# Kernel optimization log

Measured on AMD Instinct MI355X. Metric: run time of the kernel, lower is better.

## Reference

```python
import jax, jax.numpy as jnp
import numpy as np

N_NODES = 50000


def setup_inputs() -> dict:
    key = jax.random.key(0)
    k1, k2, k3, k4 = jax.random.split(key, 4)
    x = jax.random.normal(k1, (N_NODES, 256), dtype=jnp.float32)
    edge_index = jax.random.randint(k2, (2, 800000), 0, N_NODES, dtype=jnp.int64)
    W1 = jax.random.normal(k3, (256, 128), dtype=jnp.float32) * (1.0 / np.sqrt(256))
    b1 = jnp.zeros((128,), dtype=jnp.float32)
    W2 = jax.random.normal(k4, (128, 16), dtype=jnp.float32) * (1.0 / np.sqrt(128))
    b2 = jnp.zeros((16,), dtype=jnp.float32)
    return {"x": x, "edge_index": edge_index, "W1": W1, "b1": b1, "W2": W2, "b2": b2}


def _gcn_norm(edge_index, num_nodes):
    # add self-loops, then symmetric normalization D^-1/2 A D^-1/2 (PyG GCNConv default)
    loop = jnp.arange(num_nodes, dtype=edge_index.dtype)
    src = jnp.concatenate([edge_index[0], loop])
    dst = jnp.concatenate([edge_index[1], loop])
    deg = jax.ops.segment_sum(jnp.ones_like(dst, dtype=jnp.float32), dst, num_segments=num_nodes)
    dinv = jnp.where(deg > 0, jax.lax.rsqrt(deg), 0.0)
    norm = dinv[src] * dinv[dst]  # [E+N]
    return src, dst, norm


def _gcn_conv(h, W, b, src, dst, norm, num_nodes):
    h = h @ W                             # linear before propagate
    msg = h[src] * norm[:, None]          # gather + edge scaling
    agg = jax.ops.segment_sum(msg, dst, num_segments=num_nodes)  # scatter-add
    return agg + b


def reference(x, edge_index, W1, b1, W2, b2):
    n = x.shape[0]
    src, dst, norm = _gcn_norm(edge_index, n)
    h = jax.nn.relu(_gcn_conv(x, W1, b1, src, dst, norm, n))
    # F.dropout(training=False) is identity in eval mode
    out = _gcn_conv(h, W2, b2, src, dst, norm, n)
    return jax.nn.log_softmax(out, axis=1)
```

## Files before the change

kernel.cpp:

```cpp
#include <hip/hip_runtime.h>
#include <hip/hip_bf16.h>
#include <math.h>


#define FIN 256
#define FH  128
#define FO  16
#define ECH_LOG 13
#define ECH (1 << ECH_LOG)
#define NCHUNK 98
#define WPH 6272

typedef unsigned int uint;
typedef unsigned short ushort;
typedef unsigned char uchar;
typedef __attribute__((ext_vector_type(8))) short bf16x8;
typedef __attribute__((ext_vector_type(4))) float f32x4;

static __device__ __forceinline__ ushort f2bf(float f) {
    __hip_bfloat16 b = __float2bfloat16(f);
    return *reinterpret_cast<ushort*>(&b);
}
static __device__ __forceinline__ float bf2f(ushort u) {
    return __uint_as_float(((uint)u) << 16);
}

__global__ __launch_bounds__(256) void GCN_wprep_k(const float* __restrict__ W1,
                                                   ushort* __restrict__ whT,
                                                   ushort* __restrict__ wlT) {
    int i = blockIdx.x * 256 + threadIdx.x;
    int k = i >> 7, c = i & 127;
    float w = W1[i];
    ushort hh = f2bf(w);
    ushort hl = f2bf(w - bf2f(hh));
    whT[c * 256 + k] = hh;
    wlT[c * 256 + k] = hl;
}

#define G1_BR 64
#define G1_KC 32

__global__ __launch_bounds__(256, 4) void GCN_histgemm_k(
        const float* __restrict__ x, const ushort* __restrict__ whT,
        const ushort* __restrict__ wlT, ushort* __restrict__ h1,
        const int* __restrict__ edge, uint* __restrict__ cw,
        uchar* __restrict__ rank8,
        int N, int E, int nHist, int nWords, int wph) {
    __shared__ __align__(16) char smem[WPH * 4];
    int tid = threadIdx.x;

    if ((int)blockIdx.x < nHist) {
        int bid = blockIdx.x;
        int half = bid & 1;
        int c = bid >> 1;
        uint* lh = (uint*)smem;
        int w0 = half * wph;
        int wlim = nWords - w0; if (wlim > wph) wlim = wph;
        for (int j = tid; j < wlim; j += 256) lh[j] = 0;
        __syncthreads();
        int base = c << ECH_LOG;
        int lim = base + ECH; if (lim > E) lim = E;
        for (int i = base + tid; i < lim; i += 256) {
            int d = edge[E + i];
            int wd = (d >> 2) - w0;
            if ((unsigned)wd < (unsigned)wlim) {
                int sh = (d & 3) << 3;
                uint old = atomicAdd(&lh[wd], 1u << sh);
                rank8[i] = (uchar)((old >> sh) & 0xFFu);
            }
        }
        __syncthreads();
        for (int j = tid; j < wlim; j += 256)
            cw[(size_t)c * nWords + w0 + j] = lh[j];
        return;
    }

    ushort* xh_s = (ushort*)smem;
    ushort* wh_s = (ushort*)(smem + 4096);
    ushort* wl_s = (ushort*)(smem + 12288);
    int row0 = (blockIdx.x - nHist) * G1_BR;
    int ln = tid & 63;
    int w  = tid >> 6;
    int ln15 = ln & 15;
    int q16  = ln >> 4;

    f32x4 acc[4][2];
    #pragma unroll
    for (int mr = 0; mr < 4; mr++)
        #pragma unroll
        for (int nc = 0; nc < 2; nc++) acc[mr][nc] = (f32x4){0.f, 0.f, 0.f, 0.f};

    for (int kc = 0; kc < FIN; kc += G1_KC) {
        #pragma unroll
        for (int j = 0; j < 2; j++) {
            int u = tid + j * 256;
            int r = u >> 3, kq = u & 7;
            int gr = row0 + r;
            float4 v = make_float4(0.f, 0.f, 0.f, 0.f);
            if (gr < N) v = *(const float4*)&x[(size_t)gr * FIN + kc + kq * 4];
            uint2 hw;
            hw.x = (uint)f2bf(v.x) | ((uint)f2bf(v.y) << 16);
            hw.y = (uint)f2bf(v.z) | ((uint)f2bf(v.w) << 16);
            int byte = (r * 64 + kq * 8) ^ (((r >> 1) & 3) << 4);
            *(uint2*)((char*)xh_s + byte) = hw;
        }
        #pragma unroll
        for (int j = 0; j < 2; j++) {
            int u = tid + j * 256;
            int c = u >> 2, ku = u & 3;
            uint4 vh = *(const uint4*)&whT[(size_t)c * 256 + kc + ku * 8];
            uint4 vl = *(const uint4*)&wlT[(size_t)c * 256 + kc + ku * 8];
            int byte = (c * 64 + ku * 16) ^ (((c >> 1) & 3) << 4);
            *(uint4*)((char*)wh_s + byte) = vh;
            *(uint4*)((char*)wl_s + byte) = vl;
        }
        __syncthreads();

        bf16x8 ah[4], bh[2], bl[2];
        #pragma unroll
        for (int mr = 0; mr < 4; mr++) {
            int r = mr * 16 + ln15;
            int byte = r * 64 + ((q16 * 16) ^ (((r >> 1) & 3) << 4));
            ah[mr] = *(const bf16x8*)((const char*)xh_s + byte);
        }
        #pragma unroll
        for (int nc = 0; nc < 2; nc++) {
            int c = w * 32 + nc * 16 + ln15;
            int byte = c * 64 + ((q16 * 16) ^ (((c >> 1) & 3) << 4));
            bh[nc] = *(const bf16x8*)((const char*)wh_s + byte);
            bl[nc] = *(const bf16x8*)((const char*)wl_s + byte);
        }
        #pragma unroll
        for (int mr = 0; mr < 4; mr++)
            #pragma unroll
            for (int nc = 0; nc < 2; nc++) {
                acc[mr][nc] = __builtin_amdgcn_mfma_f32_16x16x32_bf16(
                    ah[mr], bh[nc], acc[mr][nc], 0, 0, 0);
                acc[mr][nc] = __builtin_amdgcn_mfma_f32_16x16x32_bf16(
                    ah[mr], bl[nc], acc[mr][nc], 0, 0, 0);
            }
        __syncthreads();
    }

    #pragma unroll
    for (int mr = 0; mr < 4; mr++) {
        #pragma unroll
        for (int nc = 0; nc < 2; nc++) {
            int cw2 = w * 32 + nc * 16 + ln15;
            #pragma unroll
            for (int j = 0; j < 4; j++) {
                int gr = row0 + mr * 16 + q16 * 4 + j;
                if (gr < N) h1[(size_t)gr * FH + cw2] = f2bf(acc[mr][nc][j]);
            }
        }
    }
}

__global__ __launch_bounds__(256) void GCN_chpfx_k(uint* __restrict__ cw,
                                                   int* __restrict__ count,
                                                   int* __restrict__ bsum,
                                                   int N, int nWords) {
    __shared__ int part[4][64][4];
    __shared__ int red[64];
    int tid = threadIdx.x;
    int wl = tid & 63, g = tid >> 6;
    int w = blockIdx.x * 64 + wl;
    int c0 = g * 25;
    int c1 = c0 + 25; if (c1 > NCHUNK) c1 = NCHUNK;

    int s0 = 0, s1 = 0, s2 = 0, s3 = 0;
    if (w < nWords) {
        for (int c = c0; c < c1; c++) {
            uint v = cw[(size_t)c * nWords + w];
            s0 += (int)(v & 0xFFu);
            s1 += (int)((v >> 8) & 0xFFu);
            s2 += (int)((v >> 16) & 0xFFu);
            s3 += (int)((v >> 24) & 0xFFu);
        }
    }
    part[g][wl][0] = s0; part[g][wl][1] = s1;
    part[g][wl][2] = s2; part[g][wl][3] = s3;
    __syncthreads();

    int b0 = 0, b1 = 0, b2 = 0, b3 = 0;
    for (int gg = 0; gg < g; gg++) {
        b0 += part[gg][wl][0]; b1 += part[gg][wl][1];
        b2 += part[gg][wl][2]; b3 += part[gg][wl][3];
    }
    if (w < nWords) {
        uint r0 = (uint)b0, r1 = (uint)b1, r2 = (uint)b2, r3 = (uint)b3;
        for (int c = c0; c < c1; c++) {
            uint* p = &cw[(size_t)c * nWords + w];
            uint v = *p;
            *p = (r0 & 0xFFu) | ((r1 & 0xFFu) << 8) | ((r2 & 0xFFu) << 16) | ((r3 & 0xFFu) << 24);
            r0 += v & 0xFFu;
            r1 += (v >> 8) & 0xFFu;
            r2 += (v >> 16) & 0xFFu;
            r3 += (v >> 24) & 0xFFu;
        }
    }
    int local = 0;
    if (g == 3 && w < nWords) {
        int t0 = b0 + s0, t1 = b1 + s1, t2 = b2 + s2, t3 = b3 + s3;
        int d0 = 4 * w;
        if (d0 + 0 < N) count[d0 + 0] = t0;
        if (d0 + 1 < N) count[d0 + 1] = t1;
        if (d0 + 2 < N) count[d0 + 2] = t2;
        if (d0 + 3 < N) count[d0 + 3] = t3;
        local = t0 + t1 + t2 + t3 + 4;
    }
    if (g == 3) red[wl] = local;
    __syncthreads();
    if (tid < 32) { red[tid] += red[tid + 32]; }
    __syncthreads();
    if (tid < 16) { red[tid] += red[tid + 16]; }
    __syncthreads();
    if (tid < 8) { red[tid] += red[tid + 8]; }
    __syncthreads();
    if (tid < 4) { red[tid] += red[tid + 4]; }
    __syncthreads();
    if (tid == 0) bsum[blockIdx.x] = red[0] + red[1] + red[2] + red[3];
}

__global__ __launch_bounds__(256) void GCN_scan2_k(const int* __restrict__ count,
                                                   const int* __restrict__ bsum,
                                                   int2* __restrict__ rd2,
                                                   uint* __restrict__ edata, int N) {
    int tid = threadIdx.x;
    int b = blockIdx.x;
    int d = b * 256 + tid;
    int cnt1 = (d < N) ? count[d] + 1 : 0;

    __shared__ int red[256];
    int offp = 0;
    for (int t = tid; t < b; t += 256) offp += bsum[t];
    red[tid] = offp;
    __syncthreads();
    for (int st = 128; st > 0; st >>= 1) {
        if (tid < st) red[tid] += red[tid + st];
        __syncthreads();
    }
    int blockOff = red[0];
    __syncthreads();

    __shared__ int ssum[256];
    ssum[tid] = cnt1;
    __syncthreads();
    for (int off = 1; off < 256; off <<= 1) {
        int t = (tid >= off) ? ssum[tid - off] : 0;
        __syncthreads();
        ssum[tid] += t;
        __syncthreads();
    }
    int r = blockOff + ssum[tid] - cnt1;

    if (d < N) {
        float dv = rsqrtf((float)cnt1);
        rd2[d] = make_int2(r, __float_as_int(dv));
        edata[r] = (uint)d | ((uint)f2bf(dv * dv) << 16);
    }
    if (b == gridDim.x - 1 && tid == 255) rd2[N] = make_int2(blockOff + ssum[255], 0);
}

__global__ __launch_bounds__(256) void GCN_fill_k(const int* __restrict__ edge,
                                                  const uchar* __restrict__ rank8,
                                                  const uint* __restrict__ cw,
                                                  const int2* __restrict__ rd2,
                                                  uint* __restrict__ edata,
                                                  int E, int nWords) {
    int i = blockIdx.x * 256 + threadIdx.x;
    if (i >= E) return;
    int s = edge[i];
    int d = edge[E + i];
    int rk = (int)rank8[i];
    int c = i >> ECH_LOG;
    uint pw = cw[(size_t)c * nWords + (d >> 2)];
    int pfx = (int)((pw >> ((d & 3) << 3)) & 0xFFu);
    int2 rdd = rd2[d];
    float ds = __int_as_float(rd2[s].y);
    float nr = ds * __int_as_float(rdd.y);
    edata[rdd.x + 1 + pfx + rk] = (uint)s | ((uint)f2bf(nr) << 16);
}

__global__ __launch_bounds__(256) void GCN_agg1gemm2_k(
        const ushort* __restrict__ h1, const int2* __restrict__ rd2,
        const uint* __restrict__ ed, const float* __restrict__ b1,
        const float* __restrict__ W2, ushort* __restrict__ h2b, int N) {
    __shared__ float w2s[FH][FO];
    __shared__ float hs[16][FH + 4];
    int tid = threadIdx.x;
    #pragma unroll
    for (int j = 0; j < (FH * FO) / 256; j++) {
        int i = tid + j * 256;
        w2s[i >> 4][i & 15] = W2[i];
    }

    int node0 = blockIdx.x * 16;
    int local = tid >> 4;
    int j = tid & 15;
    int node = node0 + local;

    if (node < N) {
        int beg = rd2[node].x, end = rd2[node + 1].x;
        const uint4* hp = (const uint4*)h1;

        float a[8];
        #pragma unroll
        for (int t = 0; t < 8; t++) a[t] = 0.f;

        int i = beg;
        for (; i + 8 <= end; i += 8) {
            uint e[8];
            uint4 gg[8];
            #pragma unroll
            for (int t = 0; t < 8; t++) e[t] = ed[i + t];
            #pragma unroll
            for (int t = 0; t < 8; t++) gg[t] = hp[(size_t)(e[t] & 0xFFFFu) * 16 + j];
            #pragma unroll
            for (int t = 0; t < 8; t++) {
                float w = bf2f((ushort)(e[t] >> 16));
                #pragma unroll
                for (int q = 0; q < 4; q++) {
                    uint u = (&gg[t].x)[q];
                    a[q*2+0] += __uint_as_float(u << 16) * w;
                    a[q*2+1] += __uint_as_float(u & 0xFFFF0000u) * w;
                }
            }
        }
        for (; i < end; i++) {
            uint e = ed[i];
            float w = bf2f((ushort)(e >> 16));
            uint4 g = hp[(size_t)(e & 0xFFFFu) * 16 + j];
            #pragma unroll
            for (int q = 0; q < 4; q++) {
                uint u = (&g.x)[q];
                a[q*2+0] += __uint_as_float(u << 16) * w;
                a[q*2+1] += __uint_as_float(u & 0xFFFF0000u) * w;
            }
        }

        const float4* bp = (const float4*)b1;
        float4 bb0 = bp[j * 2 + 0];
        float4 bb1 = bp[j * 2 + 1];
        float4 o0, o1;
        o0.x = fmaxf(a[0] + bb0.x, 0.f);
        o0.y = fmaxf(a[1] + bb0.y, 0.f);
        o0.z = fmaxf(a[2] + bb0.z, 0.f);
        o0.w = fmaxf(a[3] + bb0.w, 0.f);
        o1.x = fmaxf(a[4] + bb1.x, 0.f);
        o1.y = fmaxf(a[5] + bb1.y, 0.f);
        o1.z = fmaxf(a[6] + bb1.z, 0.f);
        o1.w = fmaxf(a[7] + bb1.w, 0.f);
        *(float4*)&hs[local][j * 8 + 0] = o0;
        *(float4*)&hs[local][j * 8 + 4] = o1;
    }
    __syncthreads();

    float acc = 0.f;
    #pragma unroll 8
    for (int k = 0; k < FH; k++) acc += hs[local][k] * w2s[k][j];
    if (node < N) h2b[(size_t)node * FO + j] = f2bf(acc);
}

__global__ __launch_bounds__(256) void GCN_agg2_k(const ushort* __restrict__ h2b,
                                                  const int2* __restrict__ rd2,
                                                  const uint* __restrict__ ed,
                                                  const float* __restrict__ b2,
                                                  float* __restrict__ out, int N) {
    int tid = threadIdx.x;
    int node = blockIdx.x * 32 + (tid >> 3);
    if (node >= N) return;
    int f2 = tid & 7;
    int beg = rd2[node].x, end = rd2[node + 1].x;
    const uint* hp = (const uint*)h2b;
    float a0 = 0.f, a1 = 0.f;
    int i = beg;
    for (; i + 8 <= end; i += 8) {
        uint e[8];
        uint u[8];
        #pragma unroll
        for (int t = 0; t < 8; t++) e[t] = ed[i + t];
        #pragma unroll
        for (int t = 0; t < 8; t++) u[t] = hp[(size_t)(e[t] & 0xFFFFu) * 8 + f2];
        #pragma unroll
        for (int t = 0; t < 8; t++) {
            float w = bf2f((ushort)(e[t] >> 16));
            a0 += __uint_as_float(u[t] << 16) * w;
            a1 += __uint_as_float(u[t] & 0xFFFF0000u) * w;
        }
    }
    for (; i < end; i++) {
        uint e = ed[i];
        uint u = hp[(size_t)(e & 0xFFFFu) * 8 + f2];
        float w = bf2f((ushort)(e >> 16));
        a0 += __uint_as_float(u << 16) * w;
        a1 += __uint_as_float(u & 0xFFFF0000u) * w;
    }
    float2 bb = ((const float2*)b2)[f2];
    float v0 = a0 + bb.x;
    float v1 = a1 + bb.y;
    float mx = fmaxf(v0, v1);
    #pragma unroll
    for (int m = 4; m >= 1; m >>= 1) mx = fmaxf(mx, __shfl_xor(mx, m, 8));
    float s = expf(v0 - mx) + expf(v1 - mx);
    #pragma unroll
    for (int m = 4; m >= 1; m >>= 1) s += __shfl_xor(s, m, 8);
    float ls = logf(s);
    float2 o = make_float2(v0 - mx - ls, v1 - mx - ls);
    ((float2*)out)[(size_t)node * 8 + f2] = o;
}

extern "C" void kernel_launch(void* const* d_in, const int* in_sizes, int n_in,
                              void* d_out, int out_size, void* d_ws, size_t ws_size,
                              hipStream_t stream) {
    (void)n_in; (void)out_size; (void)ws_size;
    const float* x  = (const float*)d_in[0];
    const int*   edp = (const int*)d_in[1];
    const float* W1 = (const float*)d_in[2];
    const float* b1 = (const float*)d_in[3];
    const float* W2 = (const float*)d_in[4];
    const float* b2 = (const float*)d_in[5];
    float* out = (float*)d_out;

    int N = in_sizes[0] / FIN;
    int E = in_sizes[1] / 2;
    int M = E + N;
    int nWords = (N + 3) / 4;
    int wph = (nWords + 1) / 2;
    int nScanBlocks = (N + 255) / 256;
    int nChpfx = (nWords + 63) / 64;

    char* p = (char*)d_ws;
    auto take = [&](size_t bytes) -> char* {
        char* r = p;
        p += (bytes + 255) & ~(size_t)255;
        return r;
    };
    int*    count  = (int*)take((size_t)N * 4);
    uchar*  rank8  = (uchar*)take((size_t)E);
    uint*   cw     = (uint*)take((size_t)NCHUNK * nWords * 4);
    int2*   rd2    = (int2*)take((size_t)(N + 1) * 8);
    int*    bsum   = (int*)take((size_t)nChpfx * 4);
    uint*   edata  = (uint*)take((size_t)M * 4);
    ushort* whT    = (ushort*)take((size_t)FH * FIN * 2);
    ushort* wlT    = (ushort*)take((size_t)FH * FIN * 2);
    ushort* h1     = (ushort*)take((size_t)N * FH * 2);
    ushort* h2b    = (ushort*)take((size_t)N * FO * 2);

    int eBlocks = (E + 255) / 256;
    int nGemm   = (N + G1_BR - 1) / G1_BR;
    int nHist   = 2 * NCHUNK;

    GCN_wprep_k<<<(FIN * FH) / 256, 256, 0, stream>>>(W1, whT, wlT);
    GCN_histgemm_k<<<nHist + nGemm, 256, 0, stream>>>(
        x, whT, wlT, h1, edp, cw, rank8, N, E, nHist, nWords, wph);
    GCN_chpfx_k<<<nChpfx, 256, 0, stream>>>(cw, count, bsum, N, nWords);
    GCN_scan2_k<<<nScanBlocks, 256, 0, stream>>>(count, bsum, rd2, edata, N);
    GCN_fill_k<<<eBlocks, 256, 0, stream>>>(edp, rank8, cw, rd2, edata, E, nWords);
    GCN_agg1gemm2_k<<<(N + 15) / 16, 256, 0, stream>>>(h1, rd2, edata, b1, W2, h2b, N);
    GCN_agg2_k<<<(N + 31) / 32, 256, 0, stream>>>(h2b, rd2, edata, b2, out, N);
}
```

Baseline: 113.1 us.

## Fuse W1 bf16 split into GEMM tile load and unroll gather loops by 16

Result: slower. 119.7 us (+5.8%).

```diff
diff --git a/kernel.cpp b/kernel.cpp
--- a/kernel.cpp
+++ b/kernel.cpp
@@ -25,24 +25,12 @@
     return __uint_as_float(((uint)u) << 16);
 }
 
-__global__ __launch_bounds__(256) void GCN_wprep_k(const float* __restrict__ W1,
-                                                   ushort* __restrict__ whT,
-                                                   ushort* __restrict__ wlT) {
-    int i = blockIdx.x * 256 + threadIdx.x;
-    int k = i >> 7, c = i & 127;
-    float w = W1[i];
-    ushort hh = f2bf(w);
-    ushort hl = f2bf(w - bf2f(hh));
-    whT[c * 256 + k] = hh;
-    wlT[c * 256 + k] = hl;
-}
-
 #define G1_BR 64
 #define G1_KC 32
 
 __global__ __launch_bounds__(256, 4) void GCN_histgemm_k(
-        const float* __restrict__ x, const ushort* __restrict__ whT,
-        const ushort* __restrict__ wlT, ushort* __restrict__ h1,
+        const float* __restrict__ x, const float* __restrict__ W1,
+        ushort* __restrict__ h1,
         const int* __restrict__ edge, uint* __restrict__ cw,
         uchar* __restrict__ rank8,
         int N, int E, int nHist, int nWords, int wph) {
@@ -105,14 +93,25 @@
             *(uint2*)((char*)xh_s + byte) = hw;
         }
         #pragma unroll
-        for (int j = 0; j < 2; j++) {
+        for (int j = 0; j < 4; j++) {
             int u = tid + j * 256;
-            int c = u >> 2, ku = u & 3;
-            uint4 vh = *(const uint4*)&whT[(size_t)c * 256 + kc + ku * 8];
-            uint4 vl = *(const uint4*)&wlT[(size_t)c * 256 + kc + ku * 8];
-            int byte = (c * 64 + ku * 16) ^ (((c >> 1) & 3) << 4);
-            *(uint4*)((char*)wh_s + byte) = vh;
-            *(uint4*)((char*)wl_s + byte) = vl;
+            int col = u & 127;
+            int k4 = (u >> 7) * 4;
+            ushort hh[4], hl[4];
+            #pragma unroll
+            for (int t = 0; t < 4; t++) {
+                float v = W1[(size_t)(kc + k4 + t) * FH + col];
+                hh[t] = f2bf(v);
+                hl[t] = f2bf(v - bf2f(hh[t]));
+            }
+            uint2 hv, lv;
+            hv.x = (uint)hh[0] | ((uint)hh[1] << 16);
+            hv.y = (uint)hh[2] | ((uint)hh[3] << 16);
+            lv.x = (uint)hl[0] | ((uint)hl[1] << 16);
+            lv.y = (uint)hl[2] | ((uint)hl[3] << 16);
+            int byte = (col * 64 + k4 * 2) ^ (((col >> 1) & 3) << 4);
+            *(uint2*)((char*)wh_s + byte) = hv;
+            *(uint2*)((char*)wl_s + byte) = lv;
         }
         __syncthreads();
 
@@ -309,6 +308,24 @@
         for (int t = 0; t < 8; t++) a[t] = 0.f;
 
         int i = beg;
+        for (; i + 16 <= end; i += 16) {
+            uint e[16];
+            uint4 gg[16];
+            #pragma unroll
+            for (int t = 0; t < 16; t++) e[t] = ed[i + t];
+            #pragma unroll
+            for (int t = 0; t < 16; t++) gg[t] = hp[(size_t)(e[t] & 0xFFFFu) * 16 + j];
+            #pragma unroll
+            for (int t = 0; t < 16; t++) {
+                float w = bf2f((ushort)(e[t] >> 16));
+                #pragma unroll
+                for (int q = 0; q < 4; q++) {
+                    uint u = (&gg[t].x)[q];
+                    a[q*2+0] += __uint_as_float(u << 16) * w;
+                    a[q*2+1] += __uint_as_float(u & 0xFFFF0000u) * w;
+                }
+            }
+        }
         for (; i + 8 <= end; i += 8) {
             uint e[8];
             uint4 gg[8];
@@ -375,6 +392,20 @@
     const uint* hp = (const uint*)h2b;
     float a0 = 0.f, a1 = 0.f;
     int i = beg;
+    for (; i + 16 <= end; i += 16) {
+        uint e[16];
+        uint u[16];
+        #pragma unroll
+        for (int t = 0; t < 16; t++) e[t] = ed[i + t];
+        #pragma unroll
+        for (int t = 0; t < 16; t++) u[t] = hp[(size_t)(e[t] & 0xFFFFu) * 8 + f2];
+        #pragma unroll
+        for (int t = 0; t < 16; t++) {
+            float w = bf2f((ushort)(e[t] >> 16));
+            a0 += __uint_as_float(u[t] << 16) * w;
+            a1 += __uint_as_float(u[t] & 0xFFFF0000u) * w;
+        }
+    }
     for (; i + 8 <= end; i += 8) {
         uint e[8];
         uint u[8];
@@ -442,8 +473,6 @@
     int2*   rd2    = (int2*)take((size_t)(N + 1) * 8);
     int*    bsum   = (int*)take((size_t)nChpfx * 4);
     uint*   edata  = (uint*)take((size_t)M * 4);
-    ushort* whT    = (ushort*)take((size_t)FH * FIN * 2);
-    ushort* wlT    = (ushort*)take((size_t)FH * FIN * 2);
     ushort* h1     = (ushort*)take((size_t)N * FH * 2);
     ushort* h2b    = (ushort*)take((size_t)N * FO * 2);
 
@@ -451,9 +480,8 @@
     int nGemm   = (N + G1_BR - 1) / G1_BR;
     int nHist   = 2 * NCHUNK;
 
-    GCN_wprep_k<<<(FIN * FH) / 256, 256, 0, stream>>>(W1, whT, wlT);
     GCN_histgemm_k<<<nHist + nGemm, 256, 0, stream>>>(
-        x, whT, wlT, h1, edp, cw, rank8, N, E, nHist, nWords, wph);
+        x, W1, h1, edp, cw, rank8, N, E, nHist, nWords, wph);
     GCN_chpfx_k<<<nChpfx, 256, 0, stream>>>(cw, count, bsum, N, nWords);
     GCN_scan2_k<<<nScanBlocks, 256, 0, stream>>>(count, bsum, rd2, edata, N);
     GCN_fill_k<<<eBlocks, 256, 0, stream>>>(edp, rank8, cw, rd2, edata, E, nWords);
```
